# Kernel optimization log

Measured on AMD Instinct MI355X. Metric: run time of the kernel, lower is better.

The kernel has to match this reference:

```python
import jax, jax.numpy as jnp
import numpy as np

B = 2_097_152  # batch of (ttm, logm) option quotes
J = 5          # hidden width from hidden_sizes=[5,5,5]


def setup_inputs() -> dict:
    key = jax.random.key(0)
    ks = jax.random.split(key, 14)
    d = jnp.float32
    s = 0.01  # torch init: normal(mean=0, std=0.01)
    inp = {
        "ttm": jax.random.uniform(ks[0], (B, 1), d),
        "logm": jax.random.normal(ks[1], (B, 1), d),
        "weights_logm": jax.random.normal(ks[2], (1, J), d) * s,
        "bias_logm": jax.random.normal(ks[3], (1, J), d) * s,
        "weights_ttm": jax.random.normal(ks[4], (1, J), d) * s,
        "bias_ttm": jax.random.normal(ks[5], (1, J), d) * s,
        "weights_exp": jax.random.normal(ks[6], (J, 1), d) * s,
        "bias_exp": jax.random.normal(ks[7], (1, J), d) * s,
        # nn.Linear default init ~ U(-1/sqrt(J), 1/sqrt(J))
        "W1": jax.random.uniform(ks[8], (J, J), d, -1.0, 1.0) / np.sqrt(J),
        "b1": jax.random.uniform(ks[9], (J,), d, -1.0, 1.0) / np.sqrt(J),
        "W2": jax.random.uniform(ks[10], (J, J), d, -1.0, 1.0) / np.sqrt(J),
        "b2": jax.random.uniform(ks[11], (J,), d, -1.0, 1.0) / np.sqrt(J),
        "Wo": jax.random.uniform(ks[12], (1, J), d, -1.0, 1.0) / np.sqrt(J),
        "bo": jax.random.uniform(ks[13], (1,), d, -1.0, 1.0) / np.sqrt(J),
    }
    return inp


def _forward(ttm, logm, weights_logm, bias_logm, weights_ttm, bias_ttm,
             weights_exp, bias_exp, W1, b1, W2, b2, Wo, bo):
    # smile transform of log-moneyness: sqrt(x*tanh(x+0.5) + tanh(-x/2) + 5e-4)
    x = bias_logm + logm @ jnp.exp(weights_logm)                     # [B, J]
    term_logm = jnp.sqrt(x * jnp.tanh(x + 0.5) + jnp.tanh(-x / 2) + 0.0005)
    term_ttm = jax.nn.sigmoid(bias_ttm + ttm @ jnp.exp(weights_ttm))  # [B, J]
    h = (term_logm * term_ttm) @ jnp.exp(weights_exp) + bias_exp      # [B,1]+[1,J] -> [B, J]
    h = jax.nn.softplus(h @ W1.T + b1)
    h = jax.nn.softplus(h @ W2.T + b2)
    return h @ Wo.T + bo                                              # [B, 1]


def reference(ttm, logm, weights_logm, bias_logm, weights_ttm, bias_ttm,
              weights_exp, bias_exp, W1, b1, W2, b2, Wo, bo):
    params = (weights_logm, bias_logm, weights_ttm, bias_ttm,
              weights_exp, bias_exp, W1, b1, W2, b2, Wo, bo)

    def out_sum(t, l):
        return jnp.sum(_forward(t, l, *params))

    output = _forward(ttm, logm, *params)                 # [B, 1]
    # grad of sum(output) wrt ttm and logm (rows independent -> per-sample grads)
    grad_ttm1, grad_logm1 = jax.grad(out_sum, argnums=(0, 1))(ttm, logm)
    # second derivative wrt logm: grad of sum(grad_logm1)
    grad_logm2 = jax.grad(
        lambda l: jnp.sum(jax.grad(out_sum, argnums=1)(ttm, l))
    )(logm)
    return (output, grad_ttm1, grad_logm1, grad_logm2)
```

## Files before the change

### kernel.cpp

```cpp
#include <hip/hip_runtime.h>
#include <math.h>

#define J 5
#define LOG2E 1.4426950408889634f
#define LN2   0.6931471805599453f

#define NSEG   128
#define SMAX   16.0f
#define SEG_STRIDE 12
#define LUT_FLOATS (NSEG * SEG_STRIDE)
#define CONST_BASE LUT_FLOATS

typedef float v2f __attribute__((ext_vector_type(2)));

#if defined(__HIP_DEVICE_COMPILE__) && __has_builtin(__builtin_amdgcn_rcpf)
__device__ __forceinline__ float fastrcp(float x) { return __builtin_amdgcn_rcpf(x); }
#else
__device__ __forceinline__ float fastrcp(float x) { return 1.0f / x; }
#endif

#if defined(__HIP_DEVICE_COMPILE__) && __has_builtin(__builtin_amdgcn_rsqf)
__device__ __forceinline__ float fastrsq(float x) { return __builtin_amdgcn_rsqf(x); }
#else
__device__ __forceinline__ float fastrsq(float x) { return 1.0f / sqrtf(x); }
#endif

#if defined(__HIP_DEVICE_COMPILE__) && __has_builtin(__builtin_amdgcn_exp2f)
__device__ __forceinline__ float fexp2(float x) { return __builtin_amdgcn_exp2f(x); }
#else
__device__ __forceinline__ float fexp2(float x) { return exp2f(x); }
#endif

__device__ __forceinline__ v2f v2s(float a) { return (v2f){a, a}; }
__device__ __forceinline__ v2f vfma(v2f a, v2f b, v2f c) { return __builtin_elementwise_fma(a, b, c); }
__device__ __forceinline__ v2f vfma(v2f a, float b, v2f c) { return __builtin_elementwise_fma(a, v2s(b), c); }
__device__ __forceinline__ v2f v2exp2(v2f x) { return (v2f){fexp2(x.x), fexp2(x.y)}; }
__device__ __forceinline__ v2f v2rcp (v2f x) { return (v2f){fastrcp(x.x), fastrcp(x.y)}; }
__device__ __forceinline__ v2f v2rsq (v2f x) { return (v2f){fastrsq(x.x), fastrsq(x.y)}; }

__device__ void node_eval(float s, const float* r1, const float* c1,
                          const float* W2, const float* b2, const float* wo, float bo,
                          float& o, float& o1, float& o2, float& o3)
{
    float h[J], h1[J], h2[J], h3[J];
#pragma unroll
    for (int j = 0; j < J; ++j) {
        const float a  = fmaf(r1[j], s, c1[j]);
        const float e  = __expf(-fabsf(a));
        const float w  = fastrcp(1.0f + e);
        const float sg = (a >= 0.0f) ? w : 1.0f - w;
        const float sp = fmaxf(a, 0.0f) + __logf(1.0f + e);
        const float d1 = sg * (1.0f - sg);
        const float d2 = d1 * (1.0f - 2.0f * sg);
        const float r  = r1[j];
        h[j]  = sp;
        h1[j] = sg * r;
        h2[j] = d1 * r * r;
        h3[j] = d2 * r * r * r;
    }
    o = bo; o1 = 0.0f; o2 = 0.0f; o3 = 0.0f;
#pragma unroll
    for (int i = 0; i < J; ++i) {
        float g = b2[i], G1 = 0.0f, G2 = 0.0f, G3 = 0.0f;
#pragma unroll
        for (int j = 0; j < J; ++j) {
            const float w = W2[i * J + j];
            g  = fmaf(w, h[j],  g);
            G1 = fmaf(w, h1[j], G1);
            G2 = fmaf(w, h2[j], G2);
            G3 = fmaf(w, h3[j], G3);
        }
        const float e  = __expf(-fabsf(g));
        const float w  = fastrcp(1.0f + e);
        const float sg = (g >= 0.0f) ? w : 1.0f - w;
        const float sp = fmaxf(g, 0.0f) + __logf(1.0f + e);
        const float d1 = sg * (1.0f - sg);
        const float d2 = d1 * (1.0f - 2.0f * sg);
        o  = fmaf(wo[i], sp, o);
        o1 = fmaf(wo[i], sg * G1, o1);
        o2 = fmaf(wo[i], fmaf(d1, G1 * G1, sg * G2), o2);
        o3 = fmaf(wo[i], fmaf(d2 * G1, G1 * G1, fmaf(3.0f * d1, G1 * G2, sg * G3)), o3);
    }
}

__global__ void setup_kernel(const float* __restrict__ w_logm, const float* __restrict__ b_logm,
                             const float* __restrict__ w_ttm,  const float* __restrict__ b_ttm,
                             const float* __restrict__ w_exp,  const float* __restrict__ b_exp,
                             const float* __restrict__ W1,     const float* __restrict__ b1,
                             const float* __restrict__ W2,     const float* __restrict__ b2,
                             const float* __restrict__ Wo,     const float* __restrict__ bo,
                             float* __restrict__ c)
{
    const int k = threadIdx.x;

    if (k < J) {
        const float ewl = __expf(w_logm[k]);
        const float ewt = __expf(w_ttm[k]);
        const float ewe = __expf(w_exp[k]);
        c[CONST_BASE + 0  + k] = ewl * LOG2E;
        c[CONST_BASE + 5  + k] = b_logm[k] * LOG2E;
        c[CONST_BASE + 10 + k] = ewl;
        c[CONST_BASE + 15 + k] = -ewt * LOG2E;
        c[CONST_BASE + 20 + k] = -b_ttm[k] * LOG2E;
        c[CONST_BASE + 25 + k] = ewe;
        c[CONST_BASE + 30 + k] = ewt * ewe;
        c[CONST_BASE + 35 + k] = 0.5f * ewl;
        c[CONST_BASE + 40 + k] = 0.25f * ewl * ewl;
    }

    float r1[J], c1[J], b2r[J], wor[J], W2r[J * J];
#pragma unroll
    for (int i = 0; i < J; ++i) {
        float r = 0.0f, cc = b1[i];
#pragma unroll
        for (int j = 0; j < J; ++j) {
            const float w = W1[i * J + j];
            r += w;
            cc = fmaf(w, b_exp[j], cc);
        }
        r1[i] = r; c1[i] = cc;
        b2r[i] = b2[i]; wor[i] = Wo[i];
    }
#pragma unroll
    for (int t = 0; t < J * J; ++t) W2r[t] = W2[t];
    const float bo0 = bo[0];

    const float h  = SMAX / (float)NSEG;
    const float s0 = h * (float)k;
    float Fa0, Fa1, Fa2, Fa3, Fb0, Fb1, Fb2, Fb3;
    node_eval(s0,     r1, c1, W2r, b2r, wor, bo0, Fa0, Fa1, Fa2, Fa3);
    node_eval(s0 + h, r1, c1, W2r, b2r, wor, bo0, Fb0, Fb1, Fb2, Fb3);

    float* seg = c + k * SEG_STRIDE;
    {
        const float Da = h * Fa1, Db = h * Fb1, D = Fb0 - Fa0;
        seg[0] = Fa0; seg[1] = Da;
        seg[2] = 3.0f * D - 2.0f * Da - Db;
        seg[3] = -2.0f * D + Da + Db;
    }
    {
        const float Da = h * Fa2, Db = h * Fb2, D = Fb1 - Fa1;
        seg[4] = Fa1; seg[5] = Da;
        seg[6] = 3.0f * D - 2.0f * Da - Db;
        seg[7] = -2.0f * D + Da + Db;
    }
    {
        const float Da = h * Fa3, Db = h * Fb3, D = Fb2 - Fa2;
        seg[8]  = Fa2; seg[9]  = Da;
        seg[10] = 3.0f * D - 2.0f * Da - Db;
        seg[11] = -2.0f * D + Da + Db;
    }
}

__device__ __forceinline__ void lut_eval(const float* __restrict__ lut, float s,
                                         float& F0, float& F1, float& F2)
{
    float t = s * ((float)NSEG / SMAX);
    t = fminf(fmaxf(t, 0.0f), (float)NSEG - 0.0005f);
    const float fl = floorf(t);
    const float fr = t - fl;
    const float* cp = lut + (int)fl * SEG_STRIDE;
    const float4 A = *(const float4*)(cp);
    const float4 B = *(const float4*)(cp + 4);
    const float4 C = *(const float4*)(cp + 8);
    F0 = fmaf(fmaf(fmaf(A.w, fr, A.z), fr, A.y), fr, A.x);
    F1 = fmaf(fmaf(fmaf(B.w, fr, B.z), fr, B.y), fr, B.x);
    F2 = fmaf(fmaf(fmaf(C.w, fr, C.z), fr, C.y), fr, C.x);
}

__global__ __launch_bounds__(256, 4) void smile_main(
    const float* __restrict__ ttm, const float* __restrict__ logm,
    const float* __restrict__ c, float* __restrict__ out, int n)
{
    __shared__ __align__(16) float lut[LUT_FLOATS];

    const int tid = blockIdx.x * blockDim.x + threadIdx.x;

    float4 T4 = make_float4(0.f, 0.f, 0.f, 0.f);
    float4 L4 = make_float4(0.f, 0.f, 0.f, 0.f);
    const bool active = (tid * 4 < n);
    if (active) {
        T4 = ((const float4*)ttm)[tid];
        L4 = ((const float4*)logm)[tid];
    }

    for (int t = threadIdx.x; t < LUT_FLOATS / 4; t += 256)
        ((float4*)lut)[t] = ((const float4*)c)[t];
    __syncthreads();

    if (!active) return;

    const v2f Ta = (v2f){T4.x, T4.y}, Tb = (v2f){T4.z, T4.w};
    const v2f La = (v2f){L4.x, L4.y}, Lb = (v2f){L4.z, L4.w};

    const float* cb = c + CONST_BASE;
    float ewlb[J], blb[J], newtb[J], nbtb[J], ewe[J], wte[J], hewl[J], qe2[J];
#pragma unroll
    for (int j = 0; j < J; ++j) {
        ewlb[j]  = cb[0  + j];
        blb[j]   = cb[5  + j];
        newtb[j] = cb[15 + j];
        nbtb[j]  = cb[20 + j];
        ewe[j]   = cb[25 + j];
        wte[j]   = cb[30 + j];
        hewl[j]  = cb[35 + j];
        qe2[j]   = cb[40 + j];
    }

    v2f sa = v2s(0.0f), sLa = v2s(0.0f), sLLa = v2s(0.0f), sTa = v2s(0.0f);
    v2f sb = v2s(0.0f), sLb = v2s(0.0f), sLLb = v2s(0.0f), sTb = v2s(0.0f);
#pragma unroll
    for (int j = 0; j < J; ++j) {
        const v2f x2A = vfma(La, ewlb[j], v2s(blb[j]));
        const v2f x2B = vfma(Lb, ewlb[j], v2s(blb[j]));
        const v2f exA = v2exp2(x2A);
        const v2f exB = v2exp2(x2B);
        const v2f zA  = vfma(Ta, newtb[j], v2s(nbtb[j]));
        const v2f zB  = vfma(Tb, newtb[j], v2s(nbtb[j]));
        const v2f ezA = v2exp2(zA);
        const v2f ezB = v2exp2(zB);

        const v2f aA = vfma(exA * exA, 2.7182818284590452f, v2s(1.0f));
        const v2f aB = vfma(exB * exB, 2.7182818284590452f, v2s(1.0f));
        const v2f bA = exA + 1.0f;
        const v2f bB = exB + 1.0f;
        const v2f rabA = v2rcp(aA * bA);
        const v2f rabB = v2rcp(aB * bB);
        const v2f ttA = v2rcp(ezA + 1.0f);
        const v2f ttB = v2rcp(ezB + 1.0f);

        const v2f xA = x2A * LN2;
        const v2f xB = x2B * LN2;
        const v2f t1A = vfma(bA * rabA, -2.0f, v2s(1.0f));
        const v2f t1B = vfma(bB * rabB, -2.0f, v2s(1.0f));
        const v2f t2A = vfma(aA * rabA,  2.0f, v2s(-1.0f));
        const v2f t2B = vfma(aB * rabB,  2.0f, v2s(-1.0f));

        const v2f m1A = vfma(-t1A, t1A, v2s(1.0f));
        const v2f m1B = vfma(-t1B, t1B, v2s(1.0f));
        const v2f m2A = vfma(-t2A, t2A, v2s(1.0f));
        const v2f m2B = vfma(-t2B, t2B, v2s(1.0f));
        const v2f uA  = vfma(xA, t1A, t2A + 5.0e-4f);
        const v2f uB  = vfma(xB, t1B, t2B + 5.0e-4f);
        const v2f rA  = v2rsq(uA);
        const v2f rB  = v2rsq(uB);

        const v2f xm1A = xA * m1A;
        const v2f xm1B = xB * m1B;
        const v2f uxA  = vfma(m2A, -0.5f, t1A + xm1A);
        const v2f uxB  = vfma(m2B, -0.5f, t1B + xm1B);
        const v2f f1A  = vfma(-t1A, xm1A, m1A);
        const v2f f1B  = vfma(-t1B, xm1B, m1B);
        const v2f uxx2A = vfma(f1A, 4.0f, -(t2A * m2A));
        const v2f uxx2B = vfma(f1B, 4.0f, -(t2B * m2B));

        const v2f tlA = uA * rA;
        const v2f tlB = uB * rB;
        const v2f ruA = rA * rA;
        const v2f ruB = rB * rB;
        const v2f hhA = uxA * ruA;
        const v2f hhB = uxB * ruB;
        const v2f inner2A = vfma(-uxA, hhA, uxx2A);
        const v2f inner2B = vfma(-uxB, hhB, uxx2B);

        const v2f dttA = vfma(-ttA, ttA, ttA);
        const v2f dttB = vfma(-ttB, ttB, ttB);
        const v2f AAa  = ttA * ewe[j];
        const v2f AAb  = ttB * ewe[j];
        const v2f AAhA = AAa * hewl[j];
        const v2f AAhB = AAb * hewl[j];
        const v2f AAqA = AAa * qe2[j];
        const v2f AAqB = AAb * qe2[j];

        sa  = vfma(tlA, AAa, sa);
        sb  = vfma(tlB, AAb, sb);
        sLa = vfma(uxA * rA, AAhA, sLa);
        sLb = vfma(uxB * rB, AAhB, sLb);
        sLLa = vfma(inner2A * rA, AAqA, sLLa);
        sLLb = vfma(inner2B * rB, AAqB, sLLb);
        sTa = vfma(tlA * dttA, wte[j], sTa);
        sTb = vfma(tlB * dttB, wte[j], sTb);
    }

    float F0[4], F1[4], F2[4];
    lut_eval(lut, sa.x, F0[0], F1[0], F2[0]);
    lut_eval(lut, sa.y, F0[1], F1[1], F2[1]);
    lut_eval(lut, sb.x, F0[2], F1[2], F2[2]);
    lut_eval(lut, sb.y, F0[3], F1[3], F2[3]);

    const size_t nn = (size_t)n;
    ((float4*)(out))[tid] = make_float4(F0[0], F0[1], F0[2], F0[3]);
    ((float4*)(out + nn))[tid] =
        make_float4(sTa.x * F1[0], sTa.y * F1[1], sTb.x * F1[2], sTb.y * F1[3]);
    ((float4*)(out + 2 * nn))[tid] =
        make_float4(sLa.x * F1[0], sLa.y * F1[1], sLb.x * F1[2], sLb.y * F1[3]);
    ((float4*)(out + 3 * nn))[tid] = make_float4(
        fmaf(sLa.x * sLa.x, F2[0], sLLa.x * F1[0]),
        fmaf(sLa.y * sLa.y, F2[1], sLLa.y * F1[1]),
        fmaf(sLb.x * sLb.x, F2[2], sLLb.x * F1[2]),
        fmaf(sLb.y * sLb.y, F2[3], sLLb.y * F1[3]));
}

extern "C" void kernel_launch(void* const* d_in, const int* in_sizes, int n_in,
                              void* d_out, int out_size, void* d_ws, size_t ws_size,
                              hipStream_t stream) {
    const float* ttm    = (const float*)d_in[0];
    const float* logm   = (const float*)d_in[1];
    const float* w_logm = (const float*)d_in[2];
    const float* b_logm = (const float*)d_in[3];
    const float* w_ttm  = (const float*)d_in[4];
    const float* b_ttm  = (const float*)d_in[5];
    const float* w_exp  = (const float*)d_in[6];
    const float* b_exp  = (const float*)d_in[7];
    const float* W1     = (const float*)d_in[8];
    const float* b1     = (const float*)d_in[9];
    const float* W2     = (const float*)d_in[10];
    const float* b2     = (const float*)d_in[11];
    const float* Wo     = (const float*)d_in[12];
    const float* bo     = (const float*)d_in[13];
    float* out = (float*)d_out;
    float* cns = (float*)d_ws;

    const int n = in_sizes[0];
    setup_kernel<<<1, NSEG, 0, stream>>>(w_logm, b_logm, w_ttm, b_ttm, w_exp, b_exp,
                                         W1, b1, W2, b2, Wo, bo, cns);
    const int threads = (n + 3) / 4;
    const int blocks  = (threads + 255) / 256;
    smile_main<<<blocks, 256, 0, stream>>>(ttm, logm, cns, out, n);
}
```

Baseline: 108.5 us.

## Fuse setup kernel into main kernel, building LUT per block in shared memory

Removes the separate single-block setup kernel launch. Every block now evaluates the 129 MLP spline nodes, builds the cubic Hermite LUT in shared memory, and computes the per-feature constants itself using readfirstlane to keep them scalar. This drops a launch and the serial dependency between two kernels, but repeats the node evaluation and the exp work in each of the ~2048 blocks and adds a second barrier.

```diff
diff --git a/kernel.cpp b/kernel.cpp
--- a/kernel.cpp
+++ b/kernel.cpp
@@ -9,7 +9,6 @@
 #define SMAX   16.0f
 #define SEG_STRIDE 12
 #define LUT_FLOATS (NSEG * SEG_STRIDE)
-#define CONST_BASE LUT_FLOATS
 
 typedef float v2f __attribute__((ext_vector_type(2)));
 
@@ -30,6 +29,10 @@
 #else
 __device__ __forceinline__ float fexp2(float x) { return exp2f(x); }
 #endif
+
+__device__ __forceinline__ float rfl(float x) {
+    return __int_as_float(__builtin_amdgcn_readfirstlane(__float_as_int(x)));
+}
 
 __device__ __forceinline__ v2f v2s(float a) { return (v2f){a, a}; }
 __device__ __forceinline__ v2f vfma(v2f a, v2f b, v2f c) { return __builtin_elementwise_fma(a, b, c); }
@@ -80,75 +83,6 @@
         o1 = fmaf(wo[i], sg * G1, o1);
         o2 = fmaf(wo[i], fmaf(d1, G1 * G1, sg * G2), o2);
         o3 = fmaf(wo[i], fmaf(d2 * G1, G1 * G1, fmaf(3.0f * d1, G1 * G2, sg * G3)), o3);
-    }
-}
-
-__global__ void setup_kernel(const float* __restrict__ w_logm, const float* __restrict__ b_logm,
-                             const float* __restrict__ w_ttm,  const float* __restrict__ b_ttm,
-                             const float* __restrict__ w_exp,  const float* __restrict__ b_exp,
-                             const float* __restrict__ W1,     const float* __restrict__ b1,
-                             const float* __restrict__ W2,     const float* __restrict__ b2,
-                             const float* __restrict__ Wo,     const float* __restrict__ bo,
-                             float* __restrict__ c)
-{
-    const int k = threadIdx.x;
-
-    if (k < J) {
-        const float ewl = __expf(w_logm[k]);
-        const float ewt = __expf(w_ttm[k]);
-        const float ewe = __expf(w_exp[k]);
-        c[CONST_BASE + 0  + k] = ewl * LOG2E;
-        c[CONST_BASE + 5  + k] = b_logm[k] * LOG2E;
-        c[CONST_BASE + 10 + k] = ewl;
-        c[CONST_BASE + 15 + k] = -ewt * LOG2E;
-        c[CONST_BASE + 20 + k] = -b_ttm[k] * LOG2E;
-        c[CONST_BASE + 25 + k] = ewe;
-        c[CONST_BASE + 30 + k] = ewt * ewe;
-        c[CONST_BASE + 35 + k] = 0.5f * ewl;
-        c[CONST_BASE + 40 + k] = 0.25f * ewl * ewl;
-    }
-
-    float r1[J], c1[J], b2r[J], wor[J], W2r[J * J];
-#pragma unroll
-    for (int i = 0; i < J; ++i) {
-        float r = 0.0f, cc = b1[i];
-#pragma unroll
-        for (int j = 0; j < J; ++j) {
-            const float w = W1[i * J + j];
-            r += w;
-            cc = fmaf(w, b_exp[j], cc);
-        }
-        r1[i] = r; c1[i] = cc;
-        b2r[i] = b2[i]; wor[i] = Wo[i];
-    }
-#pragma unroll
-    for (int t = 0; t < J * J; ++t) W2r[t] = W2[t];
-    const float bo0 = bo[0];
-
-    const float h  = SMAX / (float)NSEG;
-    const float s0 = h * (float)k;
-    float Fa0, Fa1, Fa2, Fa3, Fb0, Fb1, Fb2, Fb3;
-    node_eval(s0,     r1, c1, W2r, b2r, wor, bo0, Fa0, Fa1, Fa2, Fa3);
-    node_eval(s0 + h, r1, c1, W2r, b2r, wor, bo0, Fb0, Fb1, Fb2, Fb3);
-
-    float* seg = c + k * SEG_STRIDE;
-    {
-        const float Da = h * Fa1, Db = h * Fb1, D = Fb0 - Fa0;
-        seg[0] = Fa0; seg[1] = Da;
-        seg[2] = 3.0f * D - 2.0f * Da - Db;
-        seg[3] = -2.0f * D + Da + Db;
-    }
-    {
-        const float Da = h * Fa2, Db = h * Fb2, D = Fb1 - Fa1;
-        seg[4] = Fa1; seg[5] = Da;
-        seg[6] = 3.0f * D - 2.0f * Da - Db;
-        seg[7] = -2.0f * D + Da + Db;
-    }
-    {
-        const float Da = h * Fa3, Db = h * Fb3, D = Fb2 - Fa2;
-        seg[8]  = Fa2; seg[9]  = Da;
-        seg[10] = 3.0f * D - 2.0f * Da - Db;
-        seg[11] = -2.0f * D + Da + Db;
     }
 }
 
@@ -168,10 +102,17 @@
     F2 = fmaf(fmaf(fmaf(C.w, fr, C.z), fr, C.y), fr, C.x);
 }
 
-__global__ __launch_bounds__(256, 4) void smile_main(
-    const float* __restrict__ ttm, const float* __restrict__ logm,
-    const float* __restrict__ c, float* __restrict__ out, int n)
+__global__ __launch_bounds__(256, 4) void smile_fused(
+    const float* __restrict__ ttm,    const float* __restrict__ logm,
+    const float* __restrict__ w_logm, const float* __restrict__ b_logm,
+    const float* __restrict__ w_ttm,  const float* __restrict__ b_ttm,
+    const float* __restrict__ w_exp,  const float* __restrict__ b_exp,
+    const float* __restrict__ W1,     const float* __restrict__ b1,
+    const float* __restrict__ W2,     const float* __restrict__ b2,
+    const float* __restrict__ Wo,     const float* __restrict__ bo,
+    float* __restrict__ out, int n)
 {
+    __shared__ float4 nodes[NSEG + 1];
     __shared__ __align__(16) float lut[LUT_FLOATS];
 
     const int tid = blockIdx.x * blockDim.x + threadIdx.x;
@@ -184,28 +125,75 @@
         L4 = ((const float4*)logm)[tid];
     }
 
-    for (int t = threadIdx.x; t < LUT_FLOATS / 4; t += 256)
-        ((float4*)lut)[t] = ((const float4*)c)[t];
+    if (threadIdx.x <= NSEG) {
+        float r1[J], c1[J], b2r[J], wor[J], W2r[J * J];
+#pragma unroll
+        for (int i = 0; i < J; ++i) {
+            float r = 0.0f, cc = b1[i];
+#pragma unroll
+            for (int j = 0; j < J; ++j) {
+                const float w = W1[i * J + j];
+                r += w;
+                cc = fmaf(w, b_exp[j], cc);
+            }
+            r1[i] = r; c1[i] = cc;
+            b2r[i] = b2[i]; wor[i] = Wo[i];
+        }
+#pragma unroll
+        for (int t = 0; t < J * J; ++t) W2r[t] = W2[t];
+        const float s0 = (SMAX / (float)NSEG) * (float)threadIdx.x;
+        float o, o1, o2, o3;
+        node_eval(s0, r1, c1, W2r, b2r, wor, bo[0], o, o1, o2, o3);
+        nodes[threadIdx.x] = make_float4(o, o1, o2, o3);
+    }
+    __syncthreads();
+
+    if (threadIdx.x < NSEG) {
+        const float h = SMAX / (float)NSEG;
+        const float4 A = nodes[threadIdx.x];
+        const float4 B = nodes[threadIdx.x + 1];
+        float* seg = lut + threadIdx.x * SEG_STRIDE;
+        {
+            const float Da = h * A.y, Db = h * B.y, D = B.x - A.x;
+            seg[0] = A.x; seg[1] = Da;
+            seg[2] = 3.0f * D - 2.0f * Da - Db;
+            seg[3] = -2.0f * D + Da + Db;
+        }
+        {
+            const float Da = h * A.z, Db = h * B.z, D = B.y - A.y;
+            seg[4] = A.y; seg[5] = Da;
+            seg[6] = 3.0f * D - 2.0f * Da - Db;
+            seg[7] = -2.0f * D + Da + Db;
+        }
+        {
+            const float Da = h * A.w, Db = h * B.w, D = B.z - A.z;
+            seg[8]  = A.z; seg[9]  = Da;
+            seg[10] = 3.0f * D - 2.0f * Da - Db;
+            seg[11] = -2.0f * D + Da + Db;
+        }
+    }
+
+    float ewlb[J], blb[J], newtb[J], nbtb[J], ewe[J], wte[J], hewl[J], qe2[J];
+#pragma unroll
+    for (int j = 0; j < J; ++j) {
+        const float ewl = __expf(w_logm[j]);
+        const float ewt = __expf(w_ttm[j]);
+        const float ewe_ = __expf(w_exp[j]);
+        ewlb[j]  = rfl(ewl * LOG2E);
+        blb[j]   = rfl(b_logm[j] * LOG2E);
+        newtb[j] = rfl(-ewt * LOG2E);
+        nbtb[j]  = rfl(-b_ttm[j] * LOG2E);
+        ewe[j]   = rfl(ewe_);
+        wte[j]   = rfl(ewt * ewe_);
+        hewl[j]  = rfl(0.5f * ewl);
+        qe2[j]   = rfl(0.25f * ewl * ewl);
+    }
     __syncthreads();
 
     if (!active) return;
 
     const v2f Ta = (v2f){T4.x, T4.y}, Tb = (v2f){T4.z, T4.w};
     const v2f La = (v2f){L4.x, L4.y}, Lb = (v2f){L4.z, L4.w};
-
-    const float* cb = c + CONST_BASE;
-    float ewlb[J], blb[J], newtb[J], nbtb[J], ewe[J], wte[J], hewl[J], qe2[J];
-#pragma unroll
-    for (int j = 0; j < J; ++j) {
-        ewlb[j]  = cb[0  + j];
-        blb[j]   = cb[5  + j];
-        newtb[j] = cb[15 + j];
-        nbtb[j]  = cb[20 + j];
-        ewe[j]   = cb[25 + j];
-        wte[j]   = cb[30 + j];
-        hewl[j]  = cb[35 + j];
-        qe2[j]   = cb[40 + j];
-    }
 
     v2f sa = v2s(0.0f), sLa = v2s(0.0f), sLLa = v2s(0.0f), sTa = v2s(0.0f);
     v2f sb = v2s(0.0f), sLb = v2s(0.0f), sLLb = v2s(0.0f), sTb = v2s(0.0f);
@@ -256,10 +244,8 @@
 
         const v2f tlA = uA * rA;
         const v2f tlB = uB * rB;
-        const v2f ruA = rA * rA;
-        const v2f ruB = rB * rB;
-        const v2f hhA = uxA * ruA;
-        const v2f hhB = uxB * ruB;
+        const v2f hhA = uxA * (rA * rA);
+        const v2f hhB = uxB * (rB * rB);
         const v2f inner2A = vfma(-uxA, hhA, uxx2A);
         const v2f inner2B = vfma(-uxB, hhB, uxx2B);
 
@@ -319,12 +305,11 @@
     const float* Wo     = (const float*)d_in[12];
     const float* bo     = (const float*)d_in[13];
     float* out = (float*)d_out;
-    float* cns = (float*)d_ws;
 
     const int n = in_sizes[0];
-    setup_kernel<<<1, NSEG, 0, stream>>>(w_logm, b_logm, w_ttm, b_ttm, w_exp, b_exp,
-                                         W1, b1, W2, b2, Wo, bo, cns);
     const int threads = (n + 3) / 4;
     const int blocks  = (threads + 255) / 256;
-    smile_main<<<blocks, 256, 0, stream>>>(ttm, logm, cns, out, n);
-}
+    smile_fused<<<blocks, 256, 0, stream>>>(ttm, logm, w_logm, b_logm, w_ttm, b_ttm,
+                                            w_exp, b_exp, W1, b1, W2, b2, Wo, bo,
+                                            out, n);
+}
```

After: 111.5 us. +2.8%, slower.
